# Kernel tuning notes

Measured on AMD Instinct MI355X. Metric: run time of the kernel, lower is better.

Reference implementation:

```python
import jax, jax.numpy as jnp
import numpy as np

B, L, H = 16384, 4096, 1024

def setup_inputs() -> dict:
    key = jax.random.key(0)
    k1, k2, k3, k4 = jax.random.split(key, 4)
    return {
        "bert_output": jax.random.normal(k1, (B, H), dtype=jnp.float32),
        "label_embed": jax.random.normal(k2, (L, H), dtype=jnp.float32),
        "W": jax.random.normal(k3, (L, H), dtype=jnp.float32) * (1.0 / np.sqrt(H)),
        "b": jax.random.normal(k4, (L,), dtype=jnp.float32) * 0.02,
    }

def reference(bert_output, label_embed, W, b):
    # Faithful fused form of the original double loop:
    #   logits[i, j] = (W @ (bert_output[i] + label_embed[j]) + b)[j]
    #               = W[j] . bert_output[i] + W[j] . label_embed[j] + b[j]
    # [B,H] @ [H,L] -> [B,L]
    cross = jnp.einsum('bh,lh->bl', bert_output, W)
    # per-label diagonal term: W[j] . label_embed[j]  -> [L]
    label_bias = jnp.einsum('lh,lh->l', W, label_embed) + b
    logits = cross + label_bias[None, :]
    return logits
```

## Files before the change

kernel.cpp:

```cpp
#include <hip/hip_runtime.h>
#include <hip/hip_bf16.h>

constexpr int BDIM = 16384;
constexpr int LDIM = 4096;
constexpr int HDIM = 1024;

constexpr int BM = 256;
constexpr int BN = 256;
constexpr int BK = 64;
constexpr int KTILES = HDIM / BK;

typedef __attribute__((ext_vector_type(4))) int i32x4;

__global__ void prep_kernel(const float* __restrict__ A, const float* __restrict__ W,
                            const float* __restrict__ E, const float* __restrict__ b,
                            signed char* __restrict__ Aq, signed char* __restrict__ Wq,
                            float* __restrict__ sA, float* __restrict__ sW,
                            float* __restrict__ bias) {
  const int bid = blockIdx.x;
  const int w = threadIdx.x >> 6;
  const int l = threadIdx.x & 63;
  const bool isW = bid < (LDIM / 4);
  const int row = isW ? bid * 4 + w : (bid - LDIM / 4) * 4 + w;
  const float4* s4 = (const float4*)((isW ? W : A) + (size_t)row * HDIM);

  float4 v[4];
  float amax = 0.f, dot = 0.f;
#pragma unroll
  for (int i = 0; i < 4; ++i) {
    v[i] = s4[i * 64 + l];
    amax = fmaxf(amax, fmaxf(fmaxf(fabsf(v[i].x), fabsf(v[i].y)),
                             fmaxf(fabsf(v[i].z), fabsf(v[i].w))));
  }
  if (isW) {
    const float4* e4 = (const float4*)(E + (size_t)row * HDIM);
#pragma unroll
    for (int i = 0; i < 4; ++i) {
      float4 ev = e4[i * 64 + l];
      dot += v[i].x * ev.x + v[i].y * ev.y + v[i].z * ev.z + v[i].w * ev.w;
    }
  }
#pragma unroll
  for (int o = 32; o > 0; o >>= 1) amax = fmaxf(amax, __shfl_xor(amax, o, 64));
  if (isW) {
#pragma unroll
    for (int o = 32; o > 0; o >>= 1) dot += __shfl_xor(dot, o, 64);
  }
  const float inv = amax > 0.f ? 127.f / amax : 0.f;
  unsigned int* dst =
      (unsigned int*)((isW ? Wq : Aq) + (size_t)row * HDIM);
#pragma unroll
  for (int i = 0; i < 4; ++i) {
    int q0 = (int)rintf(v[i].x * inv), q1 = (int)rintf(v[i].y * inv);
    int q2 = (int)rintf(v[i].z * inv), q3 = (int)rintf(v[i].w * inv);
    dst[i * 64 + l] =
        (q0 & 255) | ((q1 & 255) << 8) | ((q2 & 255) << 16) | ((q3 & 255) << 24);
  }
  if (l == 0) {
    if (isW) { sW[row] = amax * (1.f / 127.f); bias[row] = dot + b[row]; }
    else sA[row] = amax * (1.f / 127.f);
  }
}

__device__ __forceinline__ void gld_lds16(const void* g, void* l) {
  __builtin_amdgcn_global_load_lds(
      (const __attribute__((address_space(1))) void*)g,
      (__attribute__((address_space(3))) void*)l, 16, 0, 0);
}

#define MEMPIN asm volatile("" ::: "memory")
#define BAR __builtin_amdgcn_s_barrier()
#define LGKM0 asm volatile("s_waitcnt lgkmcnt(0)" ::: "memory")
#define VM2 asm volatile("s_waitcnt vmcnt(2)" ::: "memory")
#define VM0 asm volatile("s_waitcnt vmcnt(0)" ::: "memory")
#define VMNONE (void)0

__global__ __launch_bounds__(512, 2) void gemm_kernel(
    const signed char* __restrict__ Aq,
    const signed char* __restrict__ Wq,
    const float* __restrict__ sA,
    const float* __restrict__ sW,
    const float* __restrict__ bias,
    float* __restrict__ C)
{
  __shared__ __attribute__((aligned(128))) signed char As[2 * BM * BK];
  __shared__ __attribute__((aligned(128))) signed char Bs[2 * BN * BK];

  const int tid = threadIdx.x;
  const int w = tid >> 6;
  const int l = tid & 63;
  const int wr = w >> 2;
  const int wc = w & 3;
  const int lr = l & 15;
  const int hi = l >> 4;

  const int bid = blockIdx.x;
  const int swz = (bid & 7) * 128 + (bid >> 3);
  const int mblk = swz >> 4;
  const int nblk = swz & 15;
  const int brow = mblk * BM;
  const int bcol = nblk * BN;

  const int srow = tid >> 2;
  const int scn = (tid & 3) ^ ((tid >> 3) & 3);
  const signed char* aSrc = Aq + (size_t)(brow + srow) * HDIM + scn * 16;
  const signed char* bSrc = Wq + (size_t)(bcol + srow) * HDIM + scn * 16;

  const int c0 = (hi ^ ((lr >> 1) & 3)) * 16;
  const int rowA = wr * 128 + lr;
  const int rowB = wc * 64 + lr;

  i32x4 acc[8][4] = {};
  i32x4 aF[4], bF0[2], bF1[2];

#define ISSUE_A(d, kk)                                                         \
  { const signed char* s_ = aSrc + (kk) * BK;                                  \
    gld_lds16(s_, &As[(d) * 16384 + w * 1024]);                                \
    gld_lds16(s_ + (size_t)128 * HDIM, &As[(d) * 16384 + 8192 + w * 1024]); }
#define ISSUE_B(d, kk)                                                         \
  { const signed char* s_ = bSrc + (kk) * BK;                                  \
    gld_lds16(s_, &Bs[(d) * 16384 + w * 1024]);                                \
    gld_lds16(s_ + (size_t)128 * HDIM, &Bs[(d) * 16384 + 8192 + w * 1024]); }

#define READ_A(d, h)                                                           \
  _Pragma("unroll") for (int mi = 0; mi < 4; ++mi) {                           \
    aF[mi] = *(const i32x4*)&As[(d) * 16384 +                                  \
                                (rowA + (h) * 64 + mi * 16) * 64 + c0];        \
  }
#define READ_B(d, g, BF)                                                       \
  _Pragma("unroll") for (int ni = 0; ni < 2; ++ni) {                           \
    BF[ni] = *(const i32x4*)&Bs[(d) * 16384 +                                  \
                                (rowB + (g) * 32 + ni * 16) * 64 + c0];        \
  }

#define MQUAD(h, g, BF)                                                        \
  _Pragma("unroll") for (int mi = 0; mi < 4; ++mi) {                           \
    _Pragma("unroll") for (int ni = 0; ni < 2; ++ni) {                         \
      acc[(h) * 4 + mi][(g) * 2 + ni] = __builtin_amdgcn_mfma_i32_16x16x64_i8( \
          aF[mi], BF[ni], acc[(h) * 4 + mi][(g) * 2 + ni], 0, 0, 0);           \
    }                                                                          \
  }

#define TILE(d, tA, tB, SA, SB, VMW, LASTBAR)                                  \
  { READ_A(d, 0) READ_B(d, 0, bF0) READ_B(d, 1, bF1)                           \
    if (SA) ISSUE_A((d) ^ 1, (tA));                                            \
    MEMPIN; BAR; LGKM0;                                                        \
    __builtin_amdgcn_s_setprio(1);                                             \
    MQUAD(0, 0, bF0) MQUAD(0, 1, bF1)                                          \
    __builtin_amdgcn_s_setprio(0);                                             \
    MEMPIN; BAR;                                                               \
    READ_A(d, 1)                                                               \
    if (SB) ISSUE_B((d), (tB));                                                \
    MEMPIN; BAR; LGKM0;                                                        \
    __builtin_amdgcn_s_setprio(1);                                             \
    MQUAD(1, 1, bF1) MQUAD(1, 0, bF0)                                          \
    __builtin_amdgcn_s_setprio(0);                                             \
    VMW;                                                                       \
    if (LASTBAR) BAR;                                                          \
    MEMPIN;                                                                    \
  }

  ISSUE_A(0, 0); ISSUE_B(0, 0); ISSUE_B(1, 1);
  VM2;
  MEMPIN; BAR;

#pragma unroll 1
  for (int t = 0; t < KTILES - 2; t += 2) {
    TILE(0, t + 1, t + 2, 1, 1, VM2, 1);
    TILE(1, t + 2, t + 3, 1, 1, VM2, 1);
  }
  TILE(0, KTILES - 1, 0, 1, 0, VM0, 1);
  TILE(1, 0, 0, 0, 0, VMNONE, 0);

  float sw4[4], bv[4];
#pragma unroll
  for (int ni = 0; ni < 4; ++ni) {
    const int cc = bcol + wc * 64 + ni * 16 + lr;
    sw4[ni] = sW[cc];
    bv[ni] = bias[cc];
  }
  const int orow0 = brow + wr * 128 + hi * 4;
  const int ocol0 = bcol + wc * 64 + lr;
#pragma unroll
  for (int mi = 0; mi < 8; ++mi) {
#pragma unroll
    for (int r = 0; r < 4; ++r) {
      const float sa = sA[orow0 + mi * 16 + r];
#pragma unroll
      for (int ni = 0; ni < 4; ++ni) {
        C[(size_t)(orow0 + mi * 16 + r) * LDIM + ocol0 + ni * 16] =
            (float)acc[mi][ni][r] * (sa * sw4[ni]) + bv[ni];
      }
    }
  }
#undef TILE
#undef MQUAD
#undef READ_A
#undef READ_B
#undef ISSUE_A
#undef ISSUE_B
}

extern "C" void kernel_launch(void* const* d_in, const int* in_sizes, int n_in,
                              void* d_out, int out_size, void* d_ws, size_t ws_size,
                              hipStream_t stream) {
  const float* bert = (const float*)d_in[0];
  const float* emb  = (const float*)d_in[1];
  const float* W    = (const float*)d_in[2];
  const float* b    = (const float*)d_in[3];
  float* out = (float*)d_out;

  char* ws = (char*)d_ws;
  signed char* Aq = (signed char*)ws;
  signed char* Wq = (signed char*)(ws + (size_t)BDIM * HDIM);
  float* sAp  = (float*)(ws + (size_t)BDIM * HDIM + (size_t)LDIM * HDIM);
  float* sWp  = (float*)((char*)sAp + BDIM * sizeof(float));
  float* bias = (float*)((char*)sWp + LDIM * sizeof(float));

  hipLaunchKernelGGL(prep_kernel, dim3(LDIM / 4 + BDIM / 4), dim3(256), 0, stream,
                     bert, W, emb, b, Aq, Wq, sAp, sWp, bias);
  hipLaunchKernelGGL(gemm_kernel, dim3((BDIM / BM) * (LDIM / BN)), dim3(512), 0, stream,
                     Aq, Wq, sAp, sWp, bias, out);
}
```

Before: 139.5 us.

## Shrink GEMM N-tile to 128, use 4-stage B buffer, single barrier per tile

Halves the block N tile to 128, which halves the per-wave accumulator footprint and raises the launch-bounds occupancy target to 4 blocks per CU. The B operand moves to a 4-deep LDS ring, the A operand stays double-buffered, and each K-tile now does one 16-MFMA block with a single barrier instead of two half-tiles with three barriers. The aim is to reduce barrier and synchronisation overhead and hide latency with more resident waves. In exchange, each A tile is reused across fewer columns, so global traffic for A doubles and the grid has twice as many blocks.

```diff
diff --git a/kernel.cpp b/kernel.cpp
--- a/kernel.cpp
+++ b/kernel.cpp
@@ -6,7 +6,7 @@
 constexpr int HDIM = 1024;
 
 constexpr int BM = 256;
-constexpr int BN = 256;
+constexpr int BN = 128;
 constexpr int BK = 64;
 constexpr int KTILES = HDIM / BK;
 
@@ -47,8 +47,7 @@
     for (int o = 32; o > 0; o >>= 1) dot += __shfl_xor(dot, o, 64);
   }
   const float inv = amax > 0.f ? 127.f / amax : 0.f;
-  unsigned int* dst =
-      (unsigned int*)((isW ? Wq : Aq) + (size_t)row * HDIM);
+  unsigned int* dst = (unsigned int*)((isW ? Wq : Aq) + (size_t)row * HDIM);
 #pragma unroll
   for (int i = 0; i < 4; ++i) {
     int q0 = (int)rintf(v[i].x * inv), q1 = (int)rintf(v[i].y * inv);
@@ -69,13 +68,14 @@
 }
 
 #define MEMPIN asm volatile("" ::: "memory")
+#define SCHED0 __builtin_amdgcn_sched_barrier(0)
 #define BAR __builtin_amdgcn_s_barrier()
 #define LGKM0 asm volatile("s_waitcnt lgkmcnt(0)" ::: "memory")
-#define VM2 asm volatile("s_waitcnt vmcnt(2)" ::: "memory")
+#define VM1 asm volatile("s_waitcnt vmcnt(1)" ::: "memory")
 #define VM0 asm volatile("s_waitcnt vmcnt(0)" ::: "memory")
 #define VMNONE (void)0
 
-__global__ __launch_bounds__(512, 2) void gemm_kernel(
+__global__ __launch_bounds__(512, 4) void gemm_kernel(
     const signed char* __restrict__ Aq,
     const signed char* __restrict__ Wq,
     const float* __restrict__ sA,
@@ -84,20 +84,20 @@
     float* __restrict__ C)
 {
   __shared__ __attribute__((aligned(128))) signed char As[2 * BM * BK];
-  __shared__ __attribute__((aligned(128))) signed char Bs[2 * BN * BK];
+  __shared__ __attribute__((aligned(128))) signed char Bs[4 * BN * BK];
 
   const int tid = threadIdx.x;
   const int w = tid >> 6;
   const int l = tid & 63;
-  const int wr = w >> 2;
-  const int wc = w & 3;
+  const int wr = w >> 1;
+  const int wc = w & 1;
   const int lr = l & 15;
   const int hi = l >> 4;
 
   const int bid = blockIdx.x;
-  const int swz = (bid & 7) * 128 + (bid >> 3);
-  const int mblk = swz >> 4;
-  const int nblk = swz & 15;
+  const int swz = (bid & 7) * 256 + (bid >> 3);
+  const int mblk = swz >> 5;
+  const int nblk = swz & 31;
   const int brow = mblk * BM;
   const int bcol = nblk * BN;
 
@@ -107,70 +107,61 @@
   const signed char* bSrc = Wq + (size_t)(bcol + srow) * HDIM + scn * 16;
 
   const int c0 = (hi ^ ((lr >> 1) & 3)) * 16;
-  const int rowA = wr * 128 + lr;
+  const int rowA = wr * 64 + lr;
   const int rowB = wc * 64 + lr;
 
-  i32x4 acc[8][4] = {};
-  i32x4 aF[4], bF0[2], bF1[2];
+  i32x4 acc[4][4] = {};
+  i32x4 aF[4], bF[4];
 
 #define ISSUE_A(d, kk)                                                         \
   { const signed char* s_ = aSrc + (kk) * BK;                                  \
     gld_lds16(s_, &As[(d) * 16384 + w * 1024]);                                \
     gld_lds16(s_ + (size_t)128 * HDIM, &As[(d) * 16384 + 8192 + w * 1024]); }
-#define ISSUE_B(d, kk)                                                         \
-  { const signed char* s_ = bSrc + (kk) * BK;                                  \
-    gld_lds16(s_, &Bs[(d) * 16384 + w * 1024]);                                \
-    gld_lds16(s_ + (size_t)128 * HDIM, &Bs[(d) * 16384 + 8192 + w * 1024]); }
-
-#define READ_A(d, h)                                                           \
+#define ISSUE_B(s, kk)                                                         \
+  gld_lds16(bSrc + (kk) * BK, &Bs[(s) * 8192 + w * 1024]);
+
+#define READ_AB(d, s)                                                          \
+  _Pragma("unroll") for (int mi = 0; mi < 4; ++mi)                             \
+    aF[mi] = *(const i32x4*)&As[(d) * 16384 + (rowA + mi * 16) * 64 + c0];     \
+  _Pragma("unroll") for (int ni = 0; ni < 4; ++ni)                             \
+    bF[ni] = *(const i32x4*)&Bs[(s) * 8192 + (rowB + ni * 16) * 64 + c0];
+
+#define MFMA16                                                                 \
   _Pragma("unroll") for (int mi = 0; mi < 4; ++mi) {                           \
-    aF[mi] = *(const i32x4*)&As[(d) * 16384 +                                  \
-                                (rowA + (h) * 64 + mi * 16) * 64 + c0];        \
-  }
-#define READ_B(d, g, BF)                                                       \
-  _Pragma("unroll") for (int ni = 0; ni < 2; ++ni) {                           \
-    BF[ni] = *(const i32x4*)&Bs[(d) * 16384 +                                  \
-                                (rowB + (g) * 32 + ni * 16) * 64 + c0];        \
-  }
-
-#define MQUAD(h, g, BF)                                                        \
-  _Pragma("unroll") for (int mi = 0; mi < 4; ++mi) {                           \
-    _Pragma("unroll") for (int ni = 0; ni < 2; ++ni) {                         \
-      acc[(h) * 4 + mi][(g) * 2 + ni] = __builtin_amdgcn_mfma_i32_16x16x64_i8( \
-          aF[mi], BF[ni], acc[(h) * 4 + mi][(g) * 2 + ni], 0, 0, 0);           \
+    _Pragma("unroll") for (int ni = 0; ni < 4; ++ni) {                         \
+      acc[mi][ni] = __builtin_amdgcn_mfma_i32_16x16x64_i8(                     \
+          aF[mi], bF[ni], acc[mi][ni], 0, 0, 0);                               \
     }                                                                          \
   }
 
-#define TILE(d, tA, tB, SA, SB, VMW, LASTBAR)                                  \
-  { READ_A(d, 0) READ_B(d, 0, bF0) READ_B(d, 1, bF1)                           \
+#define TILE(d, s, SA, tA, SB, sB, tB, VMW, DOBAR)                             \
+  { READ_AB(d, s)                                                              \
     if (SA) ISSUE_A((d) ^ 1, (tA));                                            \
-    MEMPIN; BAR; LGKM0;                                                        \
+    SCHED0; LGKM0; SCHED0;                                                     \
     __builtin_amdgcn_s_setprio(1);                                             \
-    MQUAD(0, 0, bF0) MQUAD(0, 1, bF1)                                          \
+    MFMA16                                                                     \
     __builtin_amdgcn_s_setprio(0);                                             \
-    MEMPIN; BAR;                                                               \
-    READ_A(d, 1)                                                               \
-    if (SB) ISSUE_B((d), (tB));                                                \
-    MEMPIN; BAR; LGKM0;                                                        \
-    __builtin_amdgcn_s_setprio(1);                                             \
-    MQUAD(1, 1, bF1) MQUAD(1, 0, bF0)                                          \
-    __builtin_amdgcn_s_setprio(0);                                             \
-    VMW;                                                                       \
-    if (LASTBAR) BAR;                                                          \
-    MEMPIN;                                                                    \
-  }
+    SCHED0;                                                                    \
+    if (SB) ISSUE_B((sB), (tB));                                               \
+    VMW; MEMPIN;                                                               \
+    if (DOBAR) BAR;                                                            \
+    MEMPIN; }
 
   ISSUE_A(0, 0); ISSUE_B(0, 0); ISSUE_B(1, 1);
-  VM2;
+  VM1;
   MEMPIN; BAR;
 
 #pragma unroll 1
-  for (int t = 0; t < KTILES - 2; t += 2) {
-    TILE(0, t + 1, t + 2, 1, 1, VM2, 1);
-    TILE(1, t + 2, t + 3, 1, 1, VM2, 1);
-  }
-  TILE(0, KTILES - 1, 0, 1, 0, VM0, 1);
-  TILE(1, 0, 0, 0, 0, VMNONE, 0);
+  for (int t = 0; t < 12; t += 4) {
+    TILE(0, 0, 1, t + 1, 1, 2, t + 2, VM1, 1);
+    TILE(1, 1, 1, t + 2, 1, 3, t + 3, VM1, 1);
+    TILE(0, 2, 1, t + 3, 1, 0, t + 4, VM1, 1);
+    TILE(1, 3, 1, t + 4, 1, 1, t + 5, VM1, 1);
+  }
+  TILE(0, 0, 1, 13, 1, 2, 14, VM1, 1);
+  TILE(1, 1, 1, 14, 1, 3, 15, VM1, 1);
+  TILE(0, 2, 1, 15, 0, 0, 0, VM0, 1);
+  TILE(1, 3, 0, 0, 0, 0, 0, VMNONE, 0);
 
   float sw4[4], bv[4];
 #pragma unroll
@@ -179,10 +170,10 @@
     sw4[ni] = sW[cc];
     bv[ni] = bias[cc];
   }
-  const int orow0 = brow + wr * 128 + hi * 4;
+  const int orow0 = brow + wr * 64 + hi * 4;
   const int ocol0 = bcol + wc * 64 + lr;
 #pragma unroll
-  for (int mi = 0; mi < 8; ++mi) {
+  for (int mi = 0; mi < 4; ++mi) {
 #pragma unroll
     for (int r = 0; r < 4; ++r) {
       const float sa = sA[orow0 + mi * 16 + r];
@@ -194,9 +185,8 @@
     }
   }
 #undef TILE
-#undef MQUAD
-#undef READ_A
-#undef READ_B
+#undef MFMA16
+#undef READ_AB
 #undef ISSUE_A
 #undef ISSUE_B
 }
```

Result: faster. 136.0 us (-2.6%).
